# Kernel optimization log

Measured on AMD Instinct MI355X. Metric: run time of the kernel, lower is better.

Reference implementation:

```python
import jax, jax.numpy as jnp
import numpy as np

EMBED_SIZE = 1024
HEADS = 16
HEAD_DIM = EMBED_SIZE // HEADS


def setup_inputs() -> dict:
    key = jax.random.key(0)
    k1, k2, k3, k4 = jax.random.split(key, 4)
    N, L = 4, 2048
    return {
        "values": jax.random.normal(k1, (N, L, EMBED_SIZE), dtype=jnp.float32),
        "keys": jax.random.normal(k2, (N, L, EMBED_SIZE), dtype=jnp.float32),
        "query": jax.random.normal(k3, (N, L, EMBED_SIZE), dtype=jnp.float32),
        "w_out": jax.random.normal(k4, (EMBED_SIZE, EMBED_SIZE), dtype=jnp.float32) * (1.0 / np.sqrt(EMBED_SIZE)),
        "b_out": jnp.zeros((EMBED_SIZE,), dtype=jnp.float32),
    }


def reference(values, keys, query, w_out, b_out):
    N, q_len, _ = query.shape
    v_len = values.shape[1]
    k_len = keys.shape[1]
    # split heads: (N, L, H, D). NOTE: source never applies the per-head
    # q/k/v Linear layers in forward, so raw inputs are used directly.
    v = values.reshape(N, v_len, HEADS, HEAD_DIM)
    k = keys.reshape(N, k_len, HEADS, HEAD_DIM)
    q = query.reshape(N, q_len, HEADS, HEAD_DIM)
    # energy: (N, H, Q, K); scale by sqrt(embed_size) as in the source
    energy = jnp.einsum('nqhd,nkhd->nhqk', q, k)
    attn = jax.nn.softmax(energy / jnp.sqrt(jnp.float32(EMBED_SIZE)), axis=3)
    out = jnp.einsum('nhql,nlhd->nqhd', attn, v).reshape(N, q_len, EMBED_SIZE)
    # fc_out: x @ W.T + b (torch Linear convention)
    return out @ w_out.T + b_out
```

## Files before the change

kernel.cpp:

```cpp
#include <hip/hip_runtime.h>
#include <hip/hip_bf16.h>

#define NB 4
#define LSEQ 2048
#define NH 16
#define HD 64
#define EMB 1024

typedef __attribute__((ext_vector_type(8))) short bf16x8;
typedef __attribute__((ext_vector_type(4))) float f32x4;
typedef __attribute__((ext_vector_type(16))) float f32x16;
typedef __attribute__((ext_vector_type(2))) unsigned int uint2v;

__device__ __forceinline__ unsigned short f2bf(float x) {
    union { float f; unsigned u; } v; v.f = x;
    unsigned r = v.u + 0x7fff + ((v.u >> 16) & 1);
    return (unsigned short)(r >> 16);
}

__device__ __forceinline__ float exp2_fast(float x) {
#if __has_builtin(__builtin_amdgcn_exp2f)
    return __builtin_amdgcn_exp2f(x);
#else
    float r; asm("v_exp_f32 %0, %1\n\ts_nop 1" : "=v"(r) : "v"(x)); return r;
#endif
}

__device__ __forceinline__ unsigned pack_bf2(float lo, float hi) {
    union { __hip_bfloat162 h2; unsigned u; } cv;
    cv.h2 = __float22bfloat162_rn(make_float2(lo, hi));
    return cv.u;
}

__device__ __forceinline__ void plswap(unsigned &a, unsigned &b) {
#if __has_builtin(__builtin_amdgcn_permlane32_swap)
    uint2v r = __builtin_amdgcn_permlane32_swap(a, b, false, false);
    a = r[0]; b = r[1];
#else
    asm volatile("s_nop 0\n\tv_permlane32_swap_b32 %0, %1\n\ts_nop 0"
                 : "+v"(a), "+v"(b));
#endif
}

__device__ __forceinline__ void async16(void* lds, const void* g) {
    __builtin_amdgcn_global_load_lds(
        (const __attribute__((address_space(1))) unsigned int*)g,
        (__attribute__((address_space(3))) unsigned int*)lds, 16, 0, 0);
}

__global__ void wconv_kernel(const float* __restrict__ Wf, unsigned short* __restrict__ Wb) {
    int i = (blockIdx.x * 256 + threadIdx.x) * 4;
    float4 v = *(const float4*)(Wf + i);
    ushort4 o = { f2bf(v.x), f2bf(v.y), f2bf(v.z), f2bf(v.w) };
    *(ushort4*)(Wb + i) = o;
}

__global__ void prep_all(const float* __restrict__ Wf, unsigned short* __restrict__ Wb,
                         const float* __restrict__ Kf, unsigned short* __restrict__ Kb,
                         const float* __restrict__ Vf, unsigned short* __restrict__ Vt)
{
    __shared__ float T[64][65];
    const int tid = threadIdx.x;
    const int b = blockIdx.x;

    if (b < 1024) {
        int i = (b * 256 + tid) * 4;
        float4 v = *(const float4*)(Wf + i);
        ushort4 o = { f2bf(v.x), f2bf(v.y), f2bf(v.z), f2bf(v.w) };
        *(ushort4*)(Wb + i) = o;
        return;
    }
    if (b < 5120) {
        int idx = (b - 1024) * 256 + tid;
        int c   = idx & 7;
        int key = (idx >> 3) & 2047;
        int h   = (idx >> 14) & 15;
        int n   = idx >> 18;
        const float* src = Kf + (size_t)(n * LSEQ + key) * EMB + h * HD + c * 8;
        float4 a = *(const float4*)src;
        float4 bb = *(const float4*)(src + 4);
        unsigned short* dst = Kb + (((size_t)(n * NH + h) * LSEQ + key) << 6)
                                 + ((c ^ (key & 7)) << 3);
        ushort4 o0 = { f2bf(a.x), f2bf(a.y), f2bf(a.z), f2bf(a.w) };
        ushort4 o1 = { f2bf(bb.x), f2bf(bb.y), f2bf(bb.z), f2bf(bb.w) };
        *(ushort4*)dst = o0;
        *(ushort4*)(dst + 4) = o1;
        return;
    }
    {
        const int vb = b - 5120;
        const int kt = vb & 31, h = (vb >> 5) & 15, n = vb >> 9;
        const float* src = Vf + (size_t)(n * LSEQ + kt * 64) * EMB + h * HD;
        unsigned short* dst = Vt + ((size_t)vb << 12);

        for (int i = tid; i < 1024; i += 256) {
            const int key = i >> 4;
            const int c4  = (i & 15) * 4;
            const float4 v = *(const float4*)(src + (size_t)key * EMB + c4);
            T[key][c4 + 0] = v.x; T[key][c4 + 1] = v.y;
            T[key][c4 + 2] = v.z; T[key][c4 + 3] = v.w;
        }
        __syncthreads();
        for (int i = tid; i < 512; i += 256) {
            const int d = i >> 3, c = i & 7;
            ushort4 o0 = { f2bf(T[c * 8 + 0][d]), f2bf(T[c * 8 + 1][d]),
                           f2bf(T[c * 8 + 2][d]), f2bf(T[c * 8 + 3][d]) };
            ushort4 o1 = { f2bf(T[c * 8 + 4][d]), f2bf(T[c * 8 + 5][d]),
                           f2bf(T[c * 8 + 6][d]), f2bf(T[c * 8 + 7][d]) };
            unsigned short* p = dst + (d << 6) + ((c ^ (d & 7)) << 3);
            *(ushort4*)p = o0;
            *(ushort4*)(p + 4) = o1;
        }
    }
}

__global__ __launch_bounds__(256, 4)
void attn12_kernel(const float* __restrict__ Qq, const unsigned short* __restrict__ Kb,
                   const unsigned short* __restrict__ Vt, unsigned short* __restrict__ X)
{
    __shared__ unsigned short Kl[2][4096];
    __shared__ unsigned short Vl[2][4096];

    const int tid  = threadIdx.x;
    const int lane = tid & 63;
    const int w    = tid >> 6;
    const int l31  = lane & 31;
    const int hl   = lane >> 5;
    const int swz7 = lane & 7;
    const int l    = ((blockIdx.x & 7) << 7) + (blockIdx.x >> 3);
    const int nh   = l >> 4;
    const int qtile = l & 15;
    const int n = nh >> 4, h = nh & 15;
    const int qrow0 = qtile * 128 + w * 32;

    bf16x8 ones;
    #pragma unroll
    for (int e = 0; e < 8; ++e) ones[e] = (short)0x3F80;

    const float qscale = 0.03125f * 1.44269504f;
    bf16x8 qf[4];
    {
        const float* qp = Qq + (size_t)(n * LSEQ + qrow0 + l31) * EMB + h * HD + hl * 8;
        #pragma unroll
        for (int dk = 0; dk < 4; ++dk) {
            bf16x8 t;
            #pragma unroll
            for (int e = 0; e < 8; ++e) t[e] = (short)f2bf(qp[dk * 16 + e] * qscale);
            qf[dk] = t;
        }
    }

    f32x16 oaccT[2];
    f32x16 lacc;
    #pragma unroll
    for (int e = 0; e < 16; ++e) lacc[e] = 0.f;
    #pragma unroll
    for (int db = 0; db < 2; ++db)
        #pragma unroll
        for (int e = 0; e < 16; ++e) oaccT[db][e] = 0.f;

    const unsigned short* kg0 = Kb + ((size_t)nh << 17);
    const unsigned short* vg0 = Vt + ((size_t)nh << 17);
    const int t8 = tid << 3;

    async16(&Kl[0][t8],        kg0 + t8);
    async16(&Kl[0][t8 + 2048], kg0 + t8 + 2048);
    async16(&Vl[0][t8],        vg0 + t8);
    async16(&Vl[0][t8 + 2048], vg0 + t8 + 2048);
    asm volatile("s_waitcnt vmcnt(0)" ::: "memory");
    __syncthreads();

    int cur = 0;
    for (int kt = 0; kt < LSEQ / 64; ++kt) {
        if (kt + 1 < LSEQ / 64) {
            const unsigned short* kg = kg0 + ((kt + 1) << 12) + t8;
            const unsigned short* vg = vg0 + ((kt + 1) << 12) + t8;
            async16(&Kl[cur ^ 1][t8],        kg);
            async16(&Kl[cur ^ 1][t8 + 2048], kg + 2048);
            async16(&Vl[cur ^ 1][t8],        vg);
            async16(&Vl[cur ^ 1][t8 + 2048], vg + 2048);
        }

        #pragma unroll
        for (int kb = 0; kb < 2; ++kb) {
            f32x16 sk;
            #pragma unroll
            for (int e = 0; e < 16; ++e) sk[e] = 0.f;
            #pragma unroll
            for (int dk = 0; dk < 4; ++dk) {
                bf16x8 ka = *(const bf16x8*)&Kl[cur][((kb * 32 + l31) << 6) + (((2 * dk + hl) ^ swz7) << 3)];
                sk = __builtin_amdgcn_mfma_f32_32x32x16_bf16(ka, qf[dk], sk, 0, 0, 0);
            }

            float p[16];
            #pragma unroll
            for (int e = 0; e < 16; ++e) p[e] = exp2_fast(sk[e]);
            unsigned wgt[4][2];
            #pragma unroll
            for (int gg = 0; gg < 4; ++gg) {
                wgt[gg][0] = pack_bf2(p[4 * gg + 0], p[4 * gg + 1]);
                wgt[gg][1] = pack_bf2(p[4 * gg + 2], p[4 * gg + 3]);
            }
            plswap(wgt[0][0], wgt[1][0]); plswap(wgt[0][1], wgt[1][1]);
            plswap(wgt[2][0], wgt[3][0]); plswap(wgt[2][1], wgt[3][1]);

            #pragma unroll
            for (int ks = 0; ks < 2; ++ks) {
                union { unsigned u[4]; bf16x8 v; } pu;
                pu.u[0] = wgt[2 * ks + 0][0];
                pu.u[1] = wgt[2 * ks + 0][1];
                pu.u[2] = wgt[2 * ks + 1][0];
                pu.u[3] = wgt[2 * ks + 1][1];
                lacc = __builtin_amdgcn_mfma_f32_32x32x16_bf16(ones, pu.v, lacc, 0, 0, 0);
                #pragma unroll
                for (int db = 0; db < 2; ++db) {
                    bf16x8 va = *(const bf16x8*)&Vl[cur][((db * 32 + l31) << 6) + (((4 * kb + 2 * ks + hl) ^ swz7) << 3)];
                    oaccT[db] = __builtin_amdgcn_mfma_f32_32x32x16_bf16(va, pu.v, oaccT[db], 0, 0, 0);
                }
            }
        }

        asm volatile("s_waitcnt vmcnt(0)" ::: "memory");
        __syncthreads();
        cur ^= 1;
    }

    {
        const float rcp = 1.0f / lacc[0];
        unsigned ow0[4][2], ow1[4][2];
        #pragma unroll
        for (int gg = 0; gg < 4; ++gg) {
            ow0[gg][0] = pack_bf2(oaccT[0][4 * gg + 0] * rcp, oaccT[0][4 * gg + 1] * rcp);
            ow0[gg][1] = pack_bf2(oaccT[0][4 * gg + 2] * rcp, oaccT[0][4 * gg + 3] * rcp);
            ow1[gg][0] = pack_bf2(oaccT[1][4 * gg + 0] * rcp, oaccT[1][4 * gg + 1] * rcp);
            ow1[gg][1] = pack_bf2(oaccT[1][4 * gg + 2] * rcp, oaccT[1][4 * gg + 3] * rcp);
        }
        #pragma unroll
        for (int gg = 0; gg < 4; ++gg) {
            plswap(ow0[gg][0], ow1[gg][0]);
            plswap(ow0[gg][1], ow1[gg][1]);
        }
        unsigned short* xrow = X + (size_t)(n * LSEQ + qrow0 + l31) * EMB + h * HD + hl * 32;
        #pragma unroll
        for (int gg = 0; gg < 4; ++gg) {
            uint4 st = { ow0[gg][0], ow0[gg][1], ow1[gg][0], ow1[gg][1] };
            *(uint4*)(xrow + 8 * gg) = st;
        }
    }
}

#define KPAD 72
#define PPAD 72

__global__ __launch_bounds__(256, 2)
void attn_kernel(const float* __restrict__ Vv, const float* __restrict__ Kk,
                 const float* __restrict__ Qq, unsigned short* __restrict__ X)
{
    __shared__ unsigned short Klds[64 * KPAD];
    __shared__ unsigned short Vtlds[64 * KPAD];
    __shared__ unsigned short Plds[4 * 16 * PPAD];

    const int tid  = threadIdx.x;
    const int lane = tid & 63;
    const int w    = tid >> 6;
    const int l15  = lane & 15;
    const int l4   = lane >> 4;
    const int qtile = blockIdx.x;
    const int nh    = blockIdx.y;
    const int n = nh >> 4, h = nh & 15;

    bf16x8 qf[2];
    {
        const int qrow = qtile * 64 + w * 16 + l15;
        const float* qp = Qq + (size_t)(n * LSEQ + qrow) * EMB + h * HD + l4 * 8;
        for (int kk = 0; kk < 2; ++kk) {
            bf16x8 t;
            #pragma unroll
            for (int e = 0; e < 8; ++e) t[e] = (short)f2bf(qp[kk * 32 + e] * 0.03125f);
            qf[kk] = t;
        }
    }

    f32x4 oacc[4];
    #pragma unroll
    for (int f = 0; f < 4; ++f) oacc[f] = (f32x4){0.f, 0.f, 0.f, 0.f};
    float mrun[4], lrun[4];
    #pragma unroll
    for (int r = 0; r < 4; ++r) { mrun[r] = -1e30f; lrun[r] = 0.f; }

    for (int kt = 0; kt < LSEQ / 64; ++kt) {
        __syncthreads();
        for (int i = tid; i < 1024; i += 256) {
            const int row = i >> 4;
            const int c4  = (i & 15) * 4;
            const size_t gb = (size_t)(n * LSEQ + kt * 64 + row) * EMB + h * HD + c4;
            const float4 kv = *(const float4*)(Kk + gb);
            const float4 vv = *(const float4*)(Vv + gb);
            ushort4 k4 = { f2bf(kv.x), f2bf(kv.y), f2bf(kv.z), f2bf(kv.w) };
            *(ushort4*)&Klds[row * KPAD + c4] = k4;
            Vtlds[(c4 + 0) * KPAD + row] = f2bf(vv.x);
            Vtlds[(c4 + 1) * KPAD + row] = f2bf(vv.y);
            Vtlds[(c4 + 2) * KPAD + row] = f2bf(vv.z);
            Vtlds[(c4 + 3) * KPAD + row] = f2bf(vv.w);
        }
        __syncthreads();

        f32x4 s[4];
        #pragma unroll
        for (int f = 0; f < 4; ++f) {
            f32x4 acc = (f32x4){0.f, 0.f, 0.f, 0.f};
            #pragma unroll
            for (int kk = 0; kk < 2; ++kk) {
                bf16x8 kb = *(const bf16x8*)&Klds[(f * 16 + l15) * KPAD + kk * 32 + l4 * 8];
                acc = __builtin_amdgcn_mfma_f32_16x16x32_bf16(qf[kk], kb, acc, 0, 0, 0);
            }
            s[f] = acc;
        }

        float mnew[4], corr[4];
        #pragma unroll
        for (int r = 0; r < 4; ++r) {
            float m0 = fmaxf(fmaxf(s[0][r], s[1][r]), fmaxf(s[2][r], s[3][r]));
            #pragma unroll
            for (int msk = 1; msk < 16; msk <<= 1) m0 = fmaxf(m0, __shfl_xor(m0, msk));
            mnew[r] = fmaxf(mrun[r], m0);
            corr[r] = __expf(mrun[r] - mnew[r]);
        }
        float psum[4] = {0.f, 0.f, 0.f, 0.f};
        #pragma unroll
        for (int f = 0; f < 4; ++f) {
            #pragma unroll
            for (int r = 0; r < 4; ++r) {
                float p = __expf(s[f][r] - mnew[r]);
                psum[r] += p;
                Plds[(w * 16 + l4 * 4 + r) * PPAD + f * 16 + l15] = f2bf(p);
            }
        }
        #pragma unroll
        for (int r = 0; r < 4; ++r) {
            float t = psum[r];
            #pragma unroll
            for (int msk = 1; msk < 16; msk <<= 1) t += __shfl_xor(t, msk);
            lrun[r] = lrun[r] * corr[r] + t;
            mrun[r] = mnew[r];
        }
        #pragma unroll
        for (int f = 0; f < 4; ++f) {
            #pragma unroll
            for (int r = 0; r < 4; ++r) oacc[f][r] *= corr[r];
        }
        __syncthreads();

        #pragma unroll
        for (int ks = 0; ks < 2; ++ks) {
            bf16x8 pa = *(const bf16x8*)&Plds[(w * 16 + l15) * PPAD + ks * 32 + l4 * 8];
            #pragma unroll
            for (int f = 0; f < 4; ++f) {
                bf16x8 vb = *(const bf16x8*)&Vtlds[(f * 16 + l15) * KPAD + ks * 32 + l4 * 8];
                oacc[f] = __builtin_amdgcn_mfma_f32_16x16x32_bf16(pa, vb, oacc[f], 0, 0, 0);
            }
        }
    }

    #pragma unroll
    for (int f = 0; f < 4; ++f) {
        #pragma unroll
        for (int r = 0; r < 4; ++r) {
            const int qrow = qtile * 64 + w * 16 + l4 * 4 + r;
            const float o = oacc[f][r] / lrun[r];
            X[(size_t)(n * LSEQ + qrow) * EMB + h * HD + f * 16 + l15] = f2bf(o);
        }
    }
}

__global__ __launch_bounds__(256, 2)
void proj4_kernel(const unsigned short* __restrict__ X, const unsigned short* __restrict__ Wb,
                  const float* __restrict__ bias, float* __restrict__ out)
{
    __shared__ unsigned short Al[2][8192];
    __shared__ unsigned short Bl[2][8192];

    const int tid  = threadIdx.x;
    const int lane = tid & 63;
    const int w    = tid >> 6;
    const int l15  = lane & 15;
    const int l4   = lane >> 4;
    const int bid  = blockIdx.x;
    const int bm   = (bid & 7) * 8 + ((bid >> 3) & 7);
    const int bn   = bid >> 6;
    const int wr = (w >> 1) * 64;
    const int wc = (w & 1) * 64;

    f32x4 acc[4][4];
    #pragma unroll
    for (int i = 0; i < 4; ++i)
        #pragma unroll
        for (int j = 0; j < 4; ++j) acc[i][j] = (f32x4){0.f, 0.f, 0.f, 0.f};

    int srow[4], soff[4];
    #pragma unroll
    for (int j = 0; j < 4; ++j) {
        const int cid = tid + j * 256;
        srow[j] = cid >> 3;
        const int c = cid & 7;
        soff[j] = ((c ^ (srow[j] & 7)) << 3);
    }

#define PROJ_STAGE(buf, k0)                                                          \
    {                                                                                \
        _Pragma("unroll")                                                            \
        for (int j = 0; j < 4; ++j) {                                                \
            const int cid = tid + j * 256;                                           \
            async16(&Al[buf][cid << 3],                                              \
                    &X [(size_t)(bm * 128 + srow[j]) * EMB + (k0) + soff[j]]);       \
            async16(&Bl[buf][cid << 3],                                              \
                    &Wb[(size_t)(bn * 128 + srow[j]) * EMB + (k0) + soff[j]]);       \
        }                                                                            \
    }

    PROJ_STAGE(0, 0)
    asm volatile("s_waitcnt vmcnt(0)" ::: "memory");
    __syncthreads();

    int cur = 0;
    for (int k0 = 0; k0 < EMB; k0 += 64) {
        if (k0 + 64 < EMB) PROJ_STAGE(cur ^ 1, k0 + 64)

        #pragma unroll
        for (int kk = 0; kk < 2; ++kk) {
            bf16x8 af[4], bfr[4];
            #pragma unroll
            for (int i = 0; i < 4; ++i) {
                const int row = wr + i * 16 + l15;
                af[i] = *(const bf16x8*)&Al[cur][(row << 6) + (((kk * 4 + l4) ^ (row & 7)) << 3)];
            }
            #pragma unroll
            for (int j = 0; j < 4; ++j) {
                const int row = wc + j * 16 + l15;
                bfr[j] = *(const bf16x8*)&Bl[cur][(row << 6) + (((kk * 4 + l4) ^ (row & 7)) << 3)];
            }
            #pragma unroll
            for (int i = 0; i < 4; ++i)
                #pragma unroll
                for (int j = 0; j < 4; ++j)
                    acc[i][j] = __builtin_amdgcn_mfma_f32_16x16x32_bf16(af[i], bfr[j], acc[i][j], 0, 0, 0);
        }

        asm volatile("s_waitcnt vmcnt(0)" ::: "memory");
        __syncthreads();
        cur ^= 1;
    }

    #pragma unroll
    for (int i = 0; i < 4; ++i) {
        const int row = bm * 128 + wr + i * 16 + l4 * 4;
        #pragma unroll
        for (int j = 0; j < 4; ++j) {
            const int col = bn * 128 + wc + j * 16 + l15;
            const float bj = bias[col];
            #pragma unroll
            for (int r = 0; r < 4; ++r)
                out[(size_t)(row + r) * EMB + col] = acc[i][j][r] + bj;
        }
    }
}

extern "C" void kernel_launch(void* const* d_in, const int* in_sizes, int n_in,
                              void* d_out, int out_size, void* d_ws, size_t ws_size,
                              hipStream_t stream) {
    const float* Vv   = (const float*)d_in[0];
    const float* Kk   = (const float*)d_in[1];
    const float* Qq   = (const float*)d_in[2];
    const float* Wf   = (const float*)d_in[3];
    const float* bias = (const float*)d_in[4];
    float* out = (float*)d_out;

    unsigned short* X  = (unsigned short*)d_ws;
    unsigned short* Wb = (unsigned short*)((char*)d_ws + (size_t)16 * 1024 * 1024);
    const size_t need = (size_t)50 * 1024 * 1024;

    if (ws_size >= need) {
        unsigned short* Kb = (unsigned short*)((char*)d_ws + (size_t)18 * 1024 * 1024);
        unsigned short* Vt = (unsigned short*)((char*)d_ws + (size_t)34 * 1024 * 1024);
        prep_all<<<dim3(7168), 256, 0, stream>>>(Wf, Wb, Kk, Kb, Vv, Vt);
        attn12_kernel<<<dim3(1024), 256, 0, stream>>>(Qq, Kb, Vt, X);
    } else {
        wconv_kernel<<<dim3(EMB * EMB / 1024), 256, 0, stream>>>(Wf, Wb);
        attn_kernel<<<dim3(LSEQ / 64, NB * NH), 256, 0, stream>>>(Vv, Kk, Qq, X);
    }

    proj4_kernel<<<dim3(512), 256, 0, stream>>>(X, Wb, bias, out);
}
```

Measured before the change: 136.1 us.

## Load K/V fragments directly from global in MFMA layout, drop LDS staging

The prep kernel now writes K and V-transposed into a 32-key-blocked layout that matches the MFMA operand fragments, so the attention kernel reads each lane's operands straight from global memory into registers. LDS double buffering, async copies and per-tile barriers go away, and K fragments are software-prefetched one sub-tile ahead. The row-sum is now a scalar accumulation of exp values plus a cross-half shuffle, which replaces the ones-matrix MFMA. In exchange, each of the four waves reads the same K/V from L2/global on its own rather than sharing one LDS copy, which raises cache traffic and exposes load latency.

```diff
diff --git a/kernel.cpp b/kernel.cpp
--- a/kernel.cpp
+++ b/kernel.cpp
@@ -79,8 +79,8 @@
         const float* src = Kf + (size_t)(n * LSEQ + key) * EMB + h * HD + c * 8;
         float4 a = *(const float4*)src;
         float4 bb = *(const float4*)(src + 4);
-        unsigned short* dst = Kb + (((size_t)(n * NH + h) * LSEQ + key) << 6)
-                                 + ((c ^ (key & 7)) << 3);
+        unsigned short* dst = Kb + ((size_t)((n * NH + h) * 64 + (key >> 5)) << 11)
+                                 + (((c << 5) + (key & 31)) << 3);
         ushort4 o0 = { f2bf(a.x), f2bf(a.y), f2bf(a.z), f2bf(a.w) };
         ushort4 o1 = { f2bf(bb.x), f2bf(bb.y), f2bf(bb.z), f2bf(bb.w) };
         *(ushort4*)dst = o0;
@@ -91,7 +91,7 @@
         const int vb = b - 5120;
         const int kt = vb & 31, h = (vb >> 5) & 15, n = vb >> 9;
         const float* src = Vf + (size_t)(n * LSEQ + kt * 64) * EMB + h * HD;
-        unsigned short* dst = Vt + ((size_t)vb << 12);
+        (void)n; (void)h; (void)kt;
 
         for (int i = tid; i < 1024; i += 256) {
             const int key = i >> 4;
@@ -102,41 +102,87 @@
         }
         __syncthreads();
         for (int i = tid; i < 512; i += 256) {
-            const int d = i >> 3, c = i & 7;
-            ushort4 o0 = { f2bf(T[c * 8 + 0][d]), f2bf(T[c * 8 + 1][d]),
-                           f2bf(T[c * 8 + 2][d]), f2bf(T[c * 8 + 3][d]) };
-            ushort4 o1 = { f2bf(T[c * 8 + 4][d]), f2bf(T[c * 8 + 5][d]),
-                           f2bf(T[c * 8 + 6][d]), f2bf(T[c * 8 + 7][d]) };
-            unsigned short* p = dst + (d << 6) + ((c ^ (d & 7)) << 3);
+            const int d = i >> 3, half = (i >> 2) & 1, c2 = i & 3;
+            const int k0 = half * 32 + c2 * 8;
+            ushort4 o0 = { f2bf(T[k0 + 0][d]), f2bf(T[k0 + 1][d]),
+                           f2bf(T[k0 + 2][d]), f2bf(T[k0 + 3][d]) };
+            ushort4 o1 = { f2bf(T[k0 + 4][d]), f2bf(T[k0 + 5][d]),
+                           f2bf(T[k0 + 6][d]), f2bf(T[k0 + 7][d]) };
+            unsigned short* p = Vt + ((size_t)(vb * 2 + half) << 11)
+                                   + (((c2 << 6) + d) << 3);
             *(ushort4*)p = o0;
             *(ushort4*)(p + 4) = o1;
         }
     }
 }
 
+
+__device__ __forceinline__ void attn16_body(
+    const bf16x8 (&KF)[4], const unsigned short* __restrict__ vb_,
+    const bf16x8 (&qf)[4], const int hl, const int l31,
+    f32x16 (&oaccT)[2], float &lp)
+{
+    bf16x8 vf[4];
+    #pragma unroll
+    for (int i = 0; i < 4; ++i) {
+        const int ks = i >> 1, db = i & 1;
+        vf[i] = *(const bf16x8*)(vb_ + ((((ks << 1) + hl) << 6) + (db << 5) + l31) * 8);
+    }
+
+    f32x16 sk;
+    #pragma unroll
+    for (int e = 0; e < 16; ++e) sk[e] = 0.f;
+    #pragma unroll
+    for (int dk = 0; dk < 4; ++dk)
+        sk = __builtin_amdgcn_mfma_f32_32x32x16_bf16(KF[dk], qf[dk], sk, 0, 0, 0);
+
+    float p[16];
+    #pragma unroll
+    for (int e = 0; e < 16; ++e) p[e] = exp2_fast(sk[e]);
+    {
+        float t0 = (p[0] + p[1]) + (p[2] + p[3]);
+        float t1 = (p[4] + p[5]) + (p[6] + p[7]);
+        float t2 = (p[8] + p[9]) + (p[10] + p[11]);
+        float t3 = (p[12] + p[13]) + (p[14] + p[15]);
+        lp += (t0 + t1) + (t2 + t3);
+    }
+    unsigned wgt[4][2];
+    #pragma unroll
+    for (int gg = 0; gg < 4; ++gg) {
+        wgt[gg][0] = pack_bf2(p[4 * gg + 0], p[4 * gg + 1]);
+        wgt[gg][1] = pack_bf2(p[4 * gg + 2], p[4 * gg + 3]);
+    }
+    plswap(wgt[0][0], wgt[1][0]); plswap(wgt[0][1], wgt[1][1]);
+    plswap(wgt[2][0], wgt[3][0]); plswap(wgt[2][1], wgt[3][1]);
+
+    #pragma unroll
+    for (int ks = 0; ks < 2; ++ks) {
+        union { unsigned u[4]; bf16x8 v; } pu;
+        pu.u[0] = wgt[2 * ks + 0][0];
+        pu.u[1] = wgt[2 * ks + 0][1];
+        pu.u[2] = wgt[2 * ks + 1][0];
+        pu.u[3] = wgt[2 * ks + 1][1];
+        #pragma unroll
+        for (int db = 0; db < 2; ++db)
+            oaccT[db] = __builtin_amdgcn_mfma_f32_32x32x16_bf16(vf[ks * 2 + db], pu.v, oaccT[db], 0, 0, 0);
+    }
+}
+
 __global__ __launch_bounds__(256, 4)
-void attn12_kernel(const float* __restrict__ Qq, const unsigned short* __restrict__ Kb,
+void attn16_kernel(const float* __restrict__ Qq, const unsigned short* __restrict__ Kb,
                    const unsigned short* __restrict__ Vt, unsigned short* __restrict__ X)
 {
-    __shared__ unsigned short Kl[2][4096];
-    __shared__ unsigned short Vl[2][4096];
-
     const int tid  = threadIdx.x;
     const int lane = tid & 63;
     const int w    = tid >> 6;
     const int l31  = lane & 31;
     const int hl   = lane >> 5;
-    const int swz7 = lane & 7;
     const int l    = ((blockIdx.x & 7) << 7) + (blockIdx.x >> 3);
     const int nh   = l >> 4;
     const int qtile = l & 15;
     const int n = nh >> 4, h = nh & 15;
     const int qrow0 = qtile * 128 + w * 32;
 
-    bf16x8 ones;
-    #pragma unroll
-    for (int e = 0; e < 8; ++e) ones[e] = (short)0x3F80;
-
     const float qscale = 0.03125f * 1.44269504f;
     bf16x8 qf[4];
     {
@@ -151,9 +197,7 @@
     }
 
     f32x16 oaccT[2];
-    f32x16 lacc;
-    #pragma unroll
-    for (int e = 0; e < 16; ++e) lacc[e] = 0.f;
+    float lp = 0.f;
     #pragma unroll
     for (int db = 0; db < 2; ++db)
         #pragma unroll
@@ -161,72 +205,26 @@
 
     const unsigned short* kg0 = Kb + ((size_t)nh << 17);
     const unsigned short* vg0 = Vt + ((size_t)nh << 17);
-    const int t8 = tid << 3;
-
-    async16(&Kl[0][t8],        kg0 + t8);
-    async16(&Kl[0][t8 + 2048], kg0 + t8 + 2048);
-    async16(&Vl[0][t8],        vg0 + t8);
-    async16(&Vl[0][t8 + 2048], vg0 + t8 + 2048);
-    asm volatile("s_waitcnt vmcnt(0)" ::: "memory");
-    __syncthreads();
-
-    int cur = 0;
-    for (int kt = 0; kt < LSEQ / 64; ++kt) {
-        if (kt + 1 < LSEQ / 64) {
-            const unsigned short* kg = kg0 + ((kt + 1) << 12) + t8;
-            const unsigned short* vg = vg0 + ((kt + 1) << 12) + t8;
-            async16(&Kl[cur ^ 1][t8],        kg);
-            async16(&Kl[cur ^ 1][t8 + 2048], kg + 2048);
-            async16(&Vl[cur ^ 1][t8],        vg);
-            async16(&Vl[cur ^ 1][t8 + 2048], vg + 2048);
-        }
-
-        #pragma unroll
-        for (int kb = 0; kb < 2; ++kb) {
-            f32x16 sk;
-            #pragma unroll
-            for (int e = 0; e < 16; ++e) sk[e] = 0.f;
-            #pragma unroll
-            for (int dk = 0; dk < 4; ++dk) {
-                bf16x8 ka = *(const bf16x8*)&Kl[cur][((kb * 32 + l31) << 6) + (((2 * dk + hl) ^ swz7) << 3)];
-                sk = __builtin_amdgcn_mfma_f32_32x32x16_bf16(ka, qf[dk], sk, 0, 0, 0);
-            }
-
-            float p[16];
-            #pragma unroll
-            for (int e = 0; e < 16; ++e) p[e] = exp2_fast(sk[e]);
-            unsigned wgt[4][2];
-            #pragma unroll
-            for (int gg = 0; gg < 4; ++gg) {
-                wgt[gg][0] = pack_bf2(p[4 * gg + 0], p[4 * gg + 1]);
-                wgt[gg][1] = pack_bf2(p[4 * gg + 2], p[4 * gg + 3]);
-            }
-            plswap(wgt[0][0], wgt[1][0]); plswap(wgt[0][1], wgt[1][1]);
-            plswap(wgt[2][0], wgt[3][0]); plswap(wgt[2][1], wgt[3][1]);
-
-            #pragma unroll
-            for (int ks = 0; ks < 2; ++ks) {
-                union { unsigned u[4]; bf16x8 v; } pu;
-                pu.u[0] = wgt[2 * ks + 0][0];
-                pu.u[1] = wgt[2 * ks + 0][1];
-                pu.u[2] = wgt[2 * ks + 1][0];
-                pu.u[3] = wgt[2 * ks + 1][1];
-                lacc = __builtin_amdgcn_mfma_f32_32x32x16_bf16(ones, pu.v, lacc, 0, 0, 0);
-                #pragma unroll
-                for (int db = 0; db < 2; ++db) {
-                    bf16x8 va = *(const bf16x8*)&Vl[cur][((db * 32 + l31) << 6) + (((4 * kb + 2 * ks + hl) ^ swz7) << 3)];
-                    oaccT[db] = __builtin_amdgcn_mfma_f32_32x32x16_bf16(va, pu.v, oaccT[db], 0, 0, 0);
-                }
-            }
-        }
-
-        asm volatile("s_waitcnt vmcnt(0)" ::: "memory");
-        __syncthreads();
-        cur ^= 1;
+
+    bf16x8 kA[4], kB[4];
+    auto LOADK = [&](bf16x8 (&KF)[4], int tau) {
+        const unsigned short* kb_ = kg0 + ((size_t)tau << 11);
+        #pragma unroll
+        for (int dk = 0; dk < 4; ++dk)
+            KF[dk] = *(const bf16x8*)(kb_ + ((((dk << 1) + hl) << 5) + l31) * 8);
+    };
+
+    LOADK(kA, 0);
+    for (int tt = 0; tt < 32; ++tt) {
+        LOADK(kB, 2 * tt + 1);
+        attn16_body(kA, vg0 + ((size_t)(2 * tt) << 11), qf, hl, l31, oaccT, lp);
+        if (tt < 31) LOADK(kA, 2 * tt + 2);
+        attn16_body(kB, vg0 + ((size_t)(2 * tt + 1) << 11), qf, hl, l31, oaccT, lp);
     }
 
     {
-        const float rcp = 1.0f / lacc[0];
+        const float ltot = lp + __shfl_xor(lp, 32);
+        const float rcp = 1.0f / ltot;
         unsigned ow0[4][2], ow1[4][2];
         #pragma unroll
         for (int gg = 0; gg < 4; ++gg) {
@@ -483,7 +481,7 @@
         unsigned short* Kb = (unsigned short*)((char*)d_ws + (size_t)18 * 1024 * 1024);
         unsigned short* Vt = (unsigned short*)((char*)d_ws + (size_t)34 * 1024 * 1024);
         prep_all<<<dim3(7168), 256, 0, stream>>>(Wf, Wb, Kk, Kb, Vv, Vt);
-        attn12_kernel<<<dim3(1024), 256, 0, stream>>>(Qq, Kb, Vt, X);
+        attn16_kernel<<<dim3(1024), 256, 0, stream>>>(Qq, Kb, Vt, X);
     } else {
         wconv_kernel<<<dim3(EMB * EMB / 1024), 256, 0, stream>>>(Wf, Wb);
         attn_kernel<<<dim3(LSEQ / 64, NB * NH), 256, 0, stream>>>(Vv, Kk, Qq, X);
```

New measurement: 137.6 us. About the same (+1.1%).
